# Kernel optimization log

Hardware: AMD Instinct MI355X
Metric: run time of the kernel (lower is better)

The kernel has to match this reference:

```python
import jax, jax.numpy as jnp
import numpy as np
from jax import lax

BATCH = 8192
HID = 10
IN = 64
STEPS = 512
REVERSE = True


def setup_inputs() -> dict:
    key = jax.random.key(0)
    ks = jax.random.split(key, 9)
    s_in = 1.0 / np.sqrt(HID)
    return {
        "hidden": jax.random.normal(ks[0], (1, BATCH, HID), dtype=jnp.float32),
        "w_ih": jax.random.uniform(ks[1], (3 * HID, IN), jnp.float32, -s_in, s_in),
        "w_hh": jax.random.uniform(ks[2], (3 * HID, HID), jnp.float32, -s_in, s_in),
        "b_ih": jax.random.uniform(ks[3], (3 * HID,), jnp.float32, -s_in, s_in),
        "b_hh": jax.random.uniform(ks[4], (3 * HID,), jnp.float32, -s_in, s_in),
        "l1_w": jax.random.uniform(ks[5], (10, HID), jnp.float32, -s_in, s_in),
        "l1_b": jax.random.uniform(ks[6], (10,), jnp.float32, -s_in, s_in),
        "l2_w": jax.random.uniform(ks[7], (IN, 10), jnp.float32, -s_in, s_in),
        "l2_b": jax.random.uniform(ks[8], (IN,), jnp.float32, -s_in, s_in),
        "step": STEPS,
    }


def _gru_cell(h, x, w_ih, w_hh, b_ih, b_hh):
    # PyTorch GRU gate order: reset, update, new
    gi = x @ w_ih.T + b_ih  # [B, 3H]
    gh = h @ w_hh.T + b_hh  # [B, 3H]
    i_r, i_z, i_n = jnp.split(gi, 3, axis=-1)
    h_r, h_z, h_n = jnp.split(gh, 3, axis=-1)
    r = jax.nn.sigmoid(i_r + h_r)
    z = jax.nn.sigmoid(i_z + h_z)
    n = jnp.tanh(i_n + r * h_n)
    return (1.0 - z) * n + z * h


def reference(hidden, w_ih, w_hh, b_ih, b_hh, l1_w, l1_b, l2_w, l2_b, step):
    h0 = hidden[0]  # [B, H]
    B = h0.shape[0]
    x0 = jnp.zeros((B, IN), dtype=h0.dtype)  # first GRU input is zeros

    def body(carry, _):
        h, x = carry
        h_new = _gru_cell(h, x, w_ih, w_hh, b_ih, b_hh)
        o = h_new @ l1_w.T + l1_b          # l1 on GRU output
        x_next = o @ l2_w.T + l2_b         # l2 feeds next GRU step
        return (h_new, x_next), o

    _, outs = lax.scan(body, (h0, x0), None, length=step)  # [T, B, 10]
    outs = jnp.transpose(outs, (1, 0, 2))  # [B, T, 10]
    if REVERSE:
        outs = outs[:, ::-1, :]
    return outs
```

## Files before the change

kernel.cpp:

```cpp
#include <hip/hip_runtime.h>

#define HID 10
#define STEPS 512

typedef __attribute__((ext_vector_type(2))) float v2f;
typedef __attribute__((ext_vector_type(4))) float v4f;

template<int F>
static __device__ __forceinline__ float swz(float v) {
    return __int_as_float(__builtin_amdgcn_ds_swizzle(__float_as_int(v), (F << 5) | 0x10));
}

__global__ __launch_bounds__(64, 2) void gru_decoder_kernel(
    const float* __restrict__ hidden, const float* __restrict__ w_ih,
    const float* __restrict__ w_hh, const float* __restrict__ b_ih,
    const float* __restrict__ b_hh, const float* __restrict__ l1_w,
    const float* __restrict__ l1_b, const float* __restrict__ l2_w,
    const float* __restrict__ l2_b, float* __restrict__ out)
{
    __shared__ float sWx[640];
    __shared__ float sbx[64];
    __shared__ float sWgi[300];
    __shared__ float sbgi[30];
    __shared__ float sWhh[300];
    __shared__ float sH[64];

    const int lane = threadIdx.x;
    const int f    = lane & 15;
    const int g    = lane >> 4;
    const int b    = blockIdx.x * 4 + g;
    const bool ok  = (f < HID);
    const int fi   = ok ? f : 0;

    for (int e = lane; e < 640; e += 64) {
        int i = e / 10, j = e - i * 10;
        float acc = 0.f;
        #pragma unroll
        for (int k = 0; k < 10; ++k) acc += l2_w[i * 10 + k] * l1_w[k * 10 + j];
        sWx[e] = acc;
    }
    {
        float acc = l2_b[lane];
        #pragma unroll
        for (int k = 0; k < 10; ++k) acc += l2_w[lane * 10 + k] * l1_b[k];
        sbx[lane] = acc;
    }
    for (int e = lane; e < 300; e += 64) sWhh[e] = w_hh[e];
    __syncthreads();
    for (int e = lane; e < 300; e += 64) {
        int m = e / 10, j = e - m * 10;
        float acc = 0.f;
        for (int k = 0; k < 64; ++k) acc += w_ih[m * 64 + k] * sWx[k * 10 + j];
        sWgi[e] = acc;
    }
    if (lane < 30) {
        float acc = b_ih[lane];
        for (int k = 0; k < 64; ++k) acc += w_ih[lane * 64 + k] * sbx[k];
        sbgi[lane] = acc;
    }
    __syncthreads();

    const float LOG2E = 1.4426950408889634f;
    const float S2    = 2.f * LOG2E;

    v2f wr2[5], wz2[5], wi2[5], wh2[5], wo2[5];
    #pragma unroll
    for (int k2 = 0; k2 < 5; ++k2) {
        int k0 = 2 * k2, k1 = 2 * k2 + 1;
        float r0 = -(sWgi[fi * 10 + k0] + sWhh[fi * 10 + k0]) * LOG2E;
        float r1 = -(sWgi[fi * 10 + k1] + sWhh[fi * 10 + k1]) * LOG2E;
        float z0 = -(sWgi[(10 + fi) * 10 + k0] + sWhh[(10 + fi) * 10 + k0]) * LOG2E;
        float z1 = -(sWgi[(10 + fi) * 10 + k1] + sWhh[(10 + fi) * 10 + k1]) * LOG2E;
        float i0 = sWgi[(20 + fi) * 10 + k0] * S2;
        float i1 = sWgi[(20 + fi) * 10 + k1] * S2;
        float hh0 = sWhh[(20 + fi) * 10 + k0] * S2;
        float hh1 = sWhh[(20 + fi) * 10 + k1] * S2;
        float o0 = l1_w[fi * 10 + k0];
        float o1 = l1_w[fi * 10 + k1];
        wr2[k2] = ok ? v2f{r0, r1}   : v2f{0.f, 0.f};
        wz2[k2] = ok ? v2f{z0, z1}   : v2f{0.f, 0.f};
        wi2[k2] = ok ? v2f{i0, i1}   : v2f{0.f, 0.f};
        wh2[k2] = ok ? v2f{hh0, hh1} : v2f{0.f, 0.f};
        wo2[k2] = ok ? v2f{o0, o1}   : v2f{0.f, 0.f};
    }
    const float br = ok ? -(sbgi[fi] + b_hh[fi]) * LOG2E : 0.f;
    const float bz = ok ? -(sbgi[10 + fi] + b_hh[10 + fi]) * LOG2E : 0.f;
    const float bi = ok ? sbgi[20 + fi] * S2 : 0.f;
    const float bh = ok ? b_hh[20 + fi] * S2 : 0.f;
    const float bo = ok ? l1_b[fi] : 0.f;
    const v2f BR2 = {br, 0.f}, BZ2 = {bz, 0.f}, BI2 = {bi, 0.f},
              BH2 = {bh, 0.f}, BO2 = {bo, 0.f};
    const float br0_ = ok ? -(b_ih[fi] + b_hh[fi]) * LOG2E : 0.f;
    const float bz0_ = ok ? -(b_ih[10 + fi] + b_hh[10 + fi]) * LOG2E : 0.f;
    const float bni0 = ok ? b_ih[20 + fi] * S2 : 0.f;

    float h = ok ? hidden[(size_t)b * HID + f] : 0.f;

    float* pb = out + (size_t)b * (STEPS * HID) + (size_t)(STEPS - 1) * HID + f;
    float* sHrow = &sH[g * 16];

    {
        float ha[10];
        ha[0] = swz<0>(h); ha[1] = swz<1>(h); ha[2] = swz<2>(h);
        ha[3] = swz<3>(h); ha[4] = swz<4>(h); ha[5] = swz<5>(h);
        ha[6] = swz<6>(h); ha[7] = swz<7>(h); ha[8] = swz<8>(h);
        ha[9] = swz<9>(h);
        float pr = 0.f, pz = 0.f, ph = 0.f;
        #pragma unroll
        for (int k = 0; k < 10; ++k) {
            pr += sWhh[fi * 10 + k] * ha[k];
            pz += sWhh[(10 + fi) * 10 + k] * ha[k];
            ph += sWhh[(20 + fi) * 10 + k] * ha[k];
        }
        float vr = br0_ - pr * LOG2E;
        float vz = bz0_ - pz * LOG2E;
        float r = __builtin_amdgcn_rcpf(1.f + __builtin_amdgcn_exp2f(vr));
        float z = __builtin_amdgcn_rcpf(1.f + __builtin_amdgcn_exp2f(vz));
        float y = bni0 + r * (ph * S2 + bh);
        float n = 1.f - 2.f * __builtin_amdgcn_rcpf(1.f + __builtin_amdgcn_exp2f(y));
        h = ok ? (n + z * (h - n)) : 0.f;
    }

    {
        int ph = (blockIdx.x >> 3) & 3;
        if (ph & 1) __builtin_amdgcn_s_sleep(3);
        if (ph & 2) { __builtin_amdgcn_s_sleep(3); __builtin_amdgcn_s_sleep(3); }
    }

    #pragma unroll 1
    for (int t = 1; t < STEPS; ++t) {
        sHrow[f] = h;
        __builtin_amdgcn_wave_barrier();
        __builtin_amdgcn_sched_barrier(0);
        v4f q0 = *(const v4f*)(sHrow);
        v4f q1 = *(const v4f*)(sHrow + 4);
        v2f q2 = *(const v2f*)(sHrow + 8);

        v2f h2_0 = __builtin_shufflevector(q0, q0, 0, 1);
        v2f h2_1 = __builtin_shufflevector(q0, q0, 2, 3);
        v2f h2_2 = __builtin_shufflevector(q1, q1, 0, 1);
        v2f h2_3 = __builtin_shufflevector(q1, q1, 2, 3);
        v2f h2_4 = q2;

        v2f ar = wr2[0] * h2_0 + BR2;
        v2f az = wz2[0] * h2_0 + BZ2;
        v2f ai = wi2[0] * h2_0 + BI2;
        v2f ah = wh2[0] * h2_0 + BH2;
        v2f ao = wo2[0] * h2_0 + BO2;
        ar += wr2[1] * h2_1; az += wz2[1] * h2_1; ai += wi2[1] * h2_1;
        ah += wh2[1] * h2_1; ao += wo2[1] * h2_1;
        ar += wr2[2] * h2_2; az += wz2[2] * h2_2; ai += wi2[2] * h2_2;
        ah += wh2[2] * h2_2; ao += wo2[2] * h2_2;
        ar += wr2[3] * h2_3; az += wz2[3] * h2_3; ai += wi2[3] * h2_3;
        ah += wh2[3] * h2_3; ao += wo2[3] * h2_3;
        ar += wr2[4] * h2_4; az += wz2[4] * h2_4; ai += wi2[4] * h2_4;
        ah += wh2[4] * h2_4; ao += wo2[4] * h2_4;

        float arx = ar.x + ar.y;
        float azx = az.x + az.y;
        float aix = ai.x + ai.y;
        float ahx = ah.x + ah.y;
        float o   = ao.x + ao.y;

        float er = __builtin_amdgcn_exp2f(arx);
        float r  = __builtin_amdgcn_rcpf(1.f + er);
        float ez = __builtin_amdgcn_exp2f(azx);
        float y  = __builtin_fmaf(r, ahx, aix);
        float en = __builtin_amdgcn_exp2f(y);
        float p  = en * ez;
        float tt = h - ez;
        float u  = p + tt;
        float num = __builtin_fmaf(h, en, u);
        float v   = en + ez;
        float den = (p + v) + 1.f;
        h = num * __builtin_amdgcn_rcpf(den);

        if (ok) pb[0] = o;
        pb -= HID;
    }

    {
        v2f h2[5];
        h2[0] = v2f{swz<0>(h), swz<1>(h)};
        h2[1] = v2f{swz<2>(h), swz<3>(h)};
        h2[2] = v2f{swz<4>(h), swz<5>(h)};
        h2[3] = v2f{swz<6>(h), swz<7>(h)};
        h2[4] = v2f{swz<8>(h), swz<9>(h)};
        v2f ao = {bo, 0.f};
        #pragma unroll
        for (int k2 = 0; k2 < 5; ++k2) ao += wo2[k2] * h2[k2];
        if (ok) pb[0] = ao.x + ao.y;
    }
}

extern "C" void kernel_launch(void* const* d_in, const int* in_sizes, int n_in,
                              void* d_out, int out_size, void* d_ws, size_t ws_size,
                              hipStream_t stream) {
    (void)in_sizes; (void)n_in; (void)d_ws; (void)ws_size; (void)out_size;
    dim3 grid(2048), block(64);
    gru_decoder_kernel<<<grid, block, 0, stream>>>(
        (const float*)d_in[0], (const float*)d_in[1], (const float*)d_in[2],
        (const float*)d_in[3], (const float*)d_in[4], (const float*)d_in[5],
        (const float*)d_in[6], (const float*)d_in[7], (const float*)d_in[8],
        (float*)d_out);
}
```

Before: 291.3 us.

## Interleave two independent batch-row recurrences per wave to hide latency

Each 64-lane wave now advances two independent groups of batch rows (A and B) in one time loop. The two dependency chains are interleaved so one group's LDS broadcast and transcendental latency can overlap with the other's math, and the grid is halved. The staggered s_sleep start and the per-step wave barrier are dropped, and the final output projection reuses the LDS-loaded hidden state instead of swizzles. This costs more registers per wave, the launch bound drops to 1, and there are half as many waves to spread across the CUs.

```diff
diff --git a/kernel.cpp b/kernel.cpp
--- a/kernel.cpp
+++ b/kernel.cpp
@@ -11,7 +11,7 @@
     return __int_as_float(__builtin_amdgcn_ds_swizzle(__float_as_int(v), (F << 5) | 0x10));
 }
 
-__global__ __launch_bounds__(64, 2) void gru_decoder_kernel(
+__global__ __launch_bounds__(64, 1) void gru_decoder_kernel(
     const float* __restrict__ hidden, const float* __restrict__ w_ih,
     const float* __restrict__ w_hh, const float* __restrict__ b_ih,
     const float* __restrict__ b_hh, const float* __restrict__ l1_w,
@@ -23,12 +23,13 @@
     __shared__ float sWgi[300];
     __shared__ float sbgi[30];
     __shared__ float sWhh[300];
-    __shared__ float sH[64];
+    __shared__ float sH[128];
 
     const int lane = threadIdx.x;
     const int f    = lane & 15;
     const int g    = lane >> 4;
-    const int b    = blockIdx.x * 4 + g;
+    const int bA   = blockIdx.x * 8 + g;
+    const int bB   = bA + 4;
     const bool ok  = (f < HID);
     const int fi   = ok ? f : 0;
 
@@ -94,12 +95,15 @@
     const float bz0_ = ok ? -(b_ih[10 + fi] + b_hh[10 + fi]) * LOG2E : 0.f;
     const float bni0 = ok ? b_ih[20 + fi] * S2 : 0.f;
 
-    float h = ok ? hidden[(size_t)b * HID + f] : 0.f;
-
-    float* pb = out + (size_t)b * (STEPS * HID) + (size_t)(STEPS - 1) * HID + f;
-    float* sHrow = &sH[g * 16];
-
-    {
+    float hA = ok ? hidden[(size_t)bA * HID + f] : 0.f;
+    float hB = ok ? hidden[(size_t)bB * HID + f] : 0.f;
+
+    float* pbA = out + (size_t)bA * (STEPS * HID) + (size_t)(STEPS - 1) * HID + f;
+    float* pbB = out + (size_t)bB * (STEPS * HID) + (size_t)(STEPS - 1) * HID + f;
+    float* rowA = &sH[g * 16];
+    float* rowB = &sH[(4 + g) * 16];
+
+    auto peel0 = [&](float& h) {
         float ha[10];
         ha[0] = swz<0>(h); ha[1] = swz<1>(h); ha[2] = swz<2>(h);
         ha[3] = swz<3>(h); ha[4] = swz<4>(h); ha[5] = swz<5>(h);
@@ -119,29 +123,24 @@
         float y = bni0 + r * (ph * S2 + bh);
         float n = 1.f - 2.f * __builtin_amdgcn_rcpf(1.f + __builtin_amdgcn_exp2f(y));
         h = ok ? (n + z * (h - n)) : 0.f;
-    }
-
-    {
-        int ph = (blockIdx.x >> 3) & 3;
-        if (ph & 1) __builtin_amdgcn_s_sleep(3);
-        if (ph & 2) { __builtin_amdgcn_s_sleep(3); __builtin_amdgcn_s_sleep(3); }
-    }
-
-    #pragma unroll 1
-    for (int t = 1; t < STEPS; ++t) {
-        sHrow[f] = h;
-        __builtin_amdgcn_wave_barrier();
-        __builtin_amdgcn_sched_barrier(0);
-        v4f q0 = *(const v4f*)(sHrow);
-        v4f q1 = *(const v4f*)(sHrow + 4);
-        v2f q2 = *(const v2f*)(sHrow + 8);
-
+    };
+    peel0(hA);
+    peel0(hB);
+
+    rowA[f] = hA;
+    rowB[f] = hB;
+    __builtin_amdgcn_wave_barrier();
+    v4f qA0 = *(const v4f*)(rowA); v4f qA1 = *(const v4f*)(rowA + 4);
+    v2f qA2 = *(const v2f*)(rowA + 8);
+    v4f qB0 = *(const v4f*)(rowB); v4f qB1 = *(const v4f*)(rowB + 4);
+    v2f qB2 = *(const v2f*)(rowB + 8);
+
+    auto gru_step = [&](v4f q0, v4f q1, v2f q2, float& h, float& o) {
         v2f h2_0 = __builtin_shufflevector(q0, q0, 0, 1);
         v2f h2_1 = __builtin_shufflevector(q0, q0, 2, 3);
         v2f h2_2 = __builtin_shufflevector(q1, q1, 0, 1);
         v2f h2_3 = __builtin_shufflevector(q1, q1, 2, 3);
         v2f h2_4 = q2;
-
         v2f ar = wr2[0] * h2_0 + BR2;
         v2f az = wz2[0] * h2_0 + BZ2;
         v2f ai = wi2[0] * h2_0 + BI2;
@@ -155,13 +154,11 @@
         ah += wh2[3] * h2_3; ao += wo2[3] * h2_3;
         ar += wr2[4] * h2_4; az += wz2[4] * h2_4; ai += wi2[4] * h2_4;
         ah += wh2[4] * h2_4; ao += wo2[4] * h2_4;
-
         float arx = ar.x + ar.y;
         float azx = az.x + az.y;
         float aix = ai.x + ai.y;
         float ahx = ah.x + ah.y;
-        float o   = ao.x + ao.y;
-
+        o = ao.x + ao.y;
         float er = __builtin_amdgcn_exp2f(arx);
         float r  = __builtin_amdgcn_rcpf(1.f + er);
         float ez = __builtin_amdgcn_exp2f(azx);
@@ -174,22 +171,37 @@
         float v   = en + ez;
         float den = (p + v) + 1.f;
         h = num * __builtin_amdgcn_rcpf(den);
-
-        if (ok) pb[0] = o;
-        pb -= HID;
+    };
+
+    #pragma unroll 1
+    for (int t = 1; t < STEPS; ++t) {
+        float oA, oB;
+        gru_step(qA0, qA1, qA2, hA, oA);
+        rowA[f] = hA;
+        qA0 = *(const v4f*)(rowA);
+        qA1 = *(const v4f*)(rowA + 4);
+        qA2 = *(const v2f*)(rowA + 8);
+        gru_step(qB0, qB1, qB2, hB, oB);
+        rowB[f] = hB;
+        qB0 = *(const v4f*)(rowB);
+        qB1 = *(const v4f*)(rowB + 4);
+        qB2 = *(const v2f*)(rowB + 8);
+        if (ok) { pbA[0] = oA; pbB[0] = oB; }
+        pbA -= HID; pbB -= HID;
     }
 
     {
-        v2f h2[5];
-        h2[0] = v2f{swz<0>(h), swz<1>(h)};
-        h2[1] = v2f{swz<2>(h), swz<3>(h)};
-        h2[2] = v2f{swz<4>(h), swz<5>(h)};
-        h2[3] = v2f{swz<6>(h), swz<7>(h)};
-        h2[4] = v2f{swz<8>(h), swz<9>(h)};
-        v2f ao = {bo, 0.f};
-        #pragma unroll
-        for (int k2 = 0; k2 < 5; ++k2) ao += wo2[k2] * h2[k2];
-        if (ok) pb[0] = ao.x + ao.y;
+        v2f aoA = wo2[0] * __builtin_shufflevector(qA0, qA0, 0, 1) + BO2;
+        aoA += wo2[1] * __builtin_shufflevector(qA0, qA0, 2, 3);
+        aoA += wo2[2] * __builtin_shufflevector(qA1, qA1, 0, 1);
+        aoA += wo2[3] * __builtin_shufflevector(qA1, qA1, 2, 3);
+        aoA += wo2[4] * qA2;
+        v2f aoB = wo2[0] * __builtin_shufflevector(qB0, qB0, 0, 1) + BO2;
+        aoB += wo2[1] * __builtin_shufflevector(qB0, qB0, 2, 3);
+        aoB += wo2[2] * __builtin_shufflevector(qB1, qB1, 0, 1);
+        aoB += wo2[3] * __builtin_shufflevector(qB1, qB1, 2, 3);
+        aoB += wo2[4] * qB2;
+        if (ok) { pbA[0] = aoA.x + aoA.y; pbB[0] = aoB.x + aoB.y; }
     }
 }
 
@@ -197,7 +209,7 @@
                               void* d_out, int out_size, void* d_ws, size_t ws_size,
                               hipStream_t stream) {
     (void)in_sizes; (void)n_in; (void)d_ws; (void)ws_size; (void)out_size;
-    dim3 grid(2048), block(64);
+    dim3 grid(1024), block(64);
     gru_decoder_kernel<<<grid, block, 0, stream>>>(
         (const float*)d_in[0], (const float*)d_in[1], (const float*)d_in[2],
         (const float*)d_in[3], (const float*)d_in[4], (const float*)d_in[5],
```

Measured after the change: 329.7 us. +13.2%, slower.
